# Kernel optimization log

Measured on AMD Instinct MI355X. Metric: run time of the kernel, lower is better.

## Reference

```python
import jax, jax.numpy as jnp
import numpy as np

B, L, S = 32, 8192, 128  # E == S == D == 128 required by the einsum labeling

def setup_inputs() -> dict:
    key = jax.random.key(0)
    kq, kk, kv = jax.random.split(key, 3)
    queries = jax.random.normal(kq, (B, L, S), dtype=jnp.float32)
    keys = jax.random.normal(kk, (B, S, S), dtype=jnp.float32)
    values = jax.random.normal(kv, (B, S, S), dtype=jnp.float32)
    return {"queries": queries, "keys": keys, "values": values}

def reference(queries, keys, values):
    # queries: (B, L, E), keys/values: (B, S, D) with E == S == D.
    # scores_1: sum-pooled outer product term (reduced-rank additive score)
    s1 = queries.sum(-1)[:, :, None] * keys.sum(-1)[:, None, :]   # (B, L, S)
    # scores_2: q contracted against key-position axis (plain batched matmul, no transpose)
    s2 = jnp.einsum('bls,bsd->bld', queries, keys)                # (B, L, S)
    A = jax.nn.softmax(s1 + s2, axis=-1)                          # (B, L, S)
    out = jnp.einsum('bls,bsd->bld', A, values)                   # (B, L, D)
    # original returns shape (B, 1, L, D) for the 3D-input path
    return out[:, None, :, :]
```

## Files before the change

kernel.cpp:

```cpp
#include <hip/hip_runtime.h>

#define SDIM 128
#define LDIM 8192
#define BATCH 32

#define WS_KV_STRIDE 65536
#define WS_KSUM_OFF (BATCH * WS_KV_STRIDE)

typedef __attribute__((ext_vector_type(8))) _Float16 half8;
typedef __attribute__((ext_vector_type(16))) float float16;

union H8U { half8 v; _Float16 h[8]; unsigned w[4]; };
union PU { _Float16 h[2]; unsigned u; };

static __device__ __forceinline__ float16 mfma_f16(half8 a, half8 b, float16 c) {
    return __builtin_amdgcn_mfma_f32_32x32x16_f16(a, b, c, 0, 0, 0);
}

__global__ __launch_bounds__(256) void prep_kernel(
        const float* __restrict__ keys, const float* __restrict__ values,
        char* __restrict__ ws) {
    __shared__ float T[SDIM * SDIM];
    const int b = blockIdx.x >> 1;
    const int which = blockIdx.x & 1;
    const int tid = threadIdx.x;
    const float* src = (which ? values : keys) + (size_t)b * SDIM * SDIM;

    #pragma unroll
    for (int it = 0; it < 16; ++it) {
        int i = tid + it * 256;
        int r = i >> 5, c0 = (i & 31) * 4;
        float4 v = ((const float4*)src)[i];
        float f[4] = {v.x, v.y, v.z, v.w};
        #pragma unroll
        for (int k = 0; k < 4; ++k)
            T[r * SDIM + ((c0 + k + r) & 127)] = f[k];
    }
    __syncthreads();

    if (which == 0 && tid < SDIM) {
        const float4* row = (const float4*)&T[tid * SDIM];
        float s = 0.f;
        #pragma unroll
        for (int i = 0; i < 32; ++i) { float4 v = row[i]; s += v.x + v.y + v.z + v.w; }
        ((float*)(ws + WS_KSUM_OFF + b * 512))[tid] = s;
    }

    char* dst = ws + (size_t)b * WS_KV_STRIDE + (which ? 32768 : 0);
    #pragma unroll
    for (int it = 0; it < 8; ++it) {
        int entry = it * 256 + tid;
        int lane = entry & 63, ln = lane & 31, H = lane >> 5;
        int m = entry >> 9, ks = (entry >> 6) & 7;
        int r = 32 * m + ln;
        int c0 = 16 * ks + 8 * H;
        H8U o;
        #pragma unroll
        for (int i = 0; i < 8; ++i) {
            int c = c0 + i;
            o.h[i] = (_Float16)T[c * SDIM + ((r + c) & 127)];
        }
        *(half8*)(dst + entry * 16) = o.v;
    }
}

__global__ __launch_bounds__(256, 4) void attn_kernel(
        const float* __restrict__ q, const char* __restrict__ ws,
        float* __restrict__ out) {
    __shared__ char smQ[32768];
    __shared__ float qsum_s[SDIM];
    __shared__ float ksum_s[SDIM];
    const int blk = blockIdx.x;
    const int b = blk >> 6, tile = blk & 63;
    const int tid = threadIdx.x, wave = tid >> 6, lane = tid & 63;
    const int H = lane >> 5, ln = lane & 31;

    const char* wsb = ws + (size_t)b * WS_KV_STRIDE;
    const float* qblk = q + ((size_t)b * LDIM + tile * 128) * SDIM;
    float* ob = out + ((size_t)b * LDIM + tile * 128 + wave * 32) * SDIM;

    if (tid < 32)
        ((float4*)ksum_s)[tid] = ((const float4*)(ws + WS_KSUM_OFF + b * 512))[tid];

    {
        float4 bufA[4][2], bufB[4][2];
        #pragma unroll
        for (int it = 0; it < 4; ++it) {
            int idx = it * 256 + tid;
            const float* p = qblk + (idx >> 4) * SDIM + (idx & 15) * 8;
            bufA[it][0] = *(const float4*)p;
            bufA[it][1] = *(const float4*)(p + 4);
        }
        #pragma unroll
        for (int it = 0; it < 4; ++it) {
            int idx = (it + 4) * 256 + tid;
            const float* p = qblk + (idx >> 4) * SDIM + (idx & 15) * 8;
            bufB[it][0] = *(const float4*)p;
            bufB[it][1] = *(const float4*)(p + 4);
        }
        #pragma unroll
        for (int g = 0; g < 2; ++g) {
            #pragma unroll
            for (int it2 = 0; it2 < 4; ++it2) {
                int it = g * 4 + it2;
                int idx = it * 256 + tid;
                int row = idx >> 4, cc = idx & 15;
                float4 v0 = g ? bufB[it2][0] : bufA[it2][0];
                float4 v1 = g ? bufB[it2][1] : bufA[it2][1];
                float f[8] = {v0.x, v0.y, v0.z, v0.w, v1.x, v1.y, v1.z, v1.w};
                float s = f[0] + f[1] + f[2] + f[3] + f[4] + f[5] + f[6] + f[7];
                s += __shfl_xor(s, 1, 64);
                s += __shfl_xor(s, 2, 64);
                s += __shfl_xor(s, 4, 64);
                s += __shfl_xor(s, 8, 64);
                if ((tid & 15) == 0) qsum_s[row] = s;
                H8U hv;
                #pragma unroll
                for (int i = 0; i < 8; ++i) hv.h[i] = (_Float16)f[i];
                *(half8*)(smQ + row * 256 + ((cc ^ (row & 15)) * 16)) = hv.v;
            }
        }
    }
    __syncthreads();

    const char* qrp = smQ + (wave * 32 + ln) * 256;
    const char* ktp = wsb;
    const char* vtp = wsb + 32768;
    const int lo16 = lane * 16;

    float16 acc[4];
    #pragma unroll
    for (int m = 0; m < 4; ++m) acc[m] = (float16)(0.0f);

    half8 ah[2][4];
    #pragma unroll
    for (int m = 0; m < 4; ++m)
        ah[0][m] = *(const half8*)(ktp + (m * 8) * 1024 + lo16);
    #pragma unroll
    for (int ks = 0; ks < 8; ++ks) {
        const int cur = ks & 1, nxt = cur ^ 1;
        if (ks < 7) {
            #pragma unroll
            for (int m = 0; m < 4; ++m)
                ah[nxt][m] = *(const half8*)(ktp + (m * 8 + ks + 1) * 1024 + lo16);
        }
        half8 bh = *(const half8*)(qrp + ((2 * ks + H) ^ (ln & 15)) * 16);
        #pragma unroll
        for (int m = 0; m < 4; ++m) acc[m] = mfma_f16(ah[cur][m], bh, acc[m]);
    }

    half8 av[2][4];
    #pragma unroll
    for (int dm = 0; dm < 4; ++dm)
        av[0][dm] = *(const half8*)(vtp + (dm * 8) * 1024 + lo16);

    const float qs = qsum_s[wave * 32 + ln];
    #pragma unroll
    for (int m = 0; m < 4; ++m)
        #pragma unroll
        for (int g = 0; g < 4; ++g) {
            float4 k4 = *(const float4*)&ksum_s[m * 32 + g * 8 + H * 4];
            acc[m][4 * g + 0] = fmaf(k4.x, qs, acc[m][4 * g + 0]);
            acc[m][4 * g + 1] = fmaf(k4.y, qs, acc[m][4 * g + 1]);
            acc[m][4 * g + 2] = fmaf(k4.z, qs, acc[m][4 * g + 2]);
            acc[m][4 * g + 3] = fmaf(k4.w, qs, acc[m][4 * g + 3]);
        }

    float mx = -1e30f;
    #pragma unroll
    for (int m = 0; m < 4; ++m)
        #pragma unroll
        for (int r = 0; r < 16; ++r) mx = fmaxf(mx, acc[m][r]);
    mx = fmaxf(mx, __shfl_xor(mx, 32, 64));
    float sum = 0.0f;
    #pragma unroll
    for (int m = 0; m < 4; ++m)
        #pragma unroll
        for (int r = 0; r < 16; ++r) {
            float e = __expf(acc[m][r] - mx);
            acc[m][r] = e;
            sum += e;
        }
    sum += __shfl_xor(sum, 32, 64);
    const float inv = 1.0f / sum;

    unsigned pk[4][8];
    #pragma unroll
    for (int m = 0; m < 4; ++m)
        #pragma unroll
        for (int rr = 0; rr < 8; ++rr) {
            PU pu;
            pu.h[0] = (_Float16)(acc[m][2 * rr] * inv);
            pu.h[1] = (_Float16)(acc[m][2 * rr + 1] * inv);
            pk[m][rr] = pu.u;
        }

    float16 oacc[4];
    #pragma unroll
    for (int m = 0; m < 4; ++m) oacc[m] = (float16)(0.0f);

    #pragma unroll
    for (int t = 0; t < 8; ++t) {
        const int cur = t & 1, nxt = cur ^ 1;
        if (t < 7) {
            #pragma unroll
            for (int dm = 0; dm < 4; ++dm)
                av[nxt][dm] = *(const half8*)(vtp + (dm * 8 + t + 1) * 1024 + lo16);
        }
        const int m = t >> 1;
        const int c = 4 * (t & 1);
        unsigned p0 = pk[m][c], p1 = pk[m][c + 1], p2 = pk[m][c + 2], p3 = pk[m][c + 3];
        unsigned a0 = H ? p2 : p0, a1 = H ? p3 : p1;
        unsigned s0 = H ? p0 : p2, s1 = H ? p1 : p3;
        unsigned r0 = (unsigned)__shfl_xor((int)s0, 32, 64);
        unsigned r1 = (unsigned)__shfl_xor((int)s1, 32, 64);
        H8U bf;
        bf.w[0] = H ? r0 : a0;
        bf.w[1] = H ? r1 : a1;
        bf.w[2] = H ? a0 : r0;
        bf.w[3] = H ? a1 : r1;
        #pragma unroll
        for (int dm = 0; dm < 4; ++dm)
            oacc[dm] = mfma_f16(av[cur][dm], bf.v, oacc[dm]);
    }

    #pragma unroll
    for (int dm = 0; dm < 4; ++dm)
        #pragma unroll
        for (int g = 0; g < 4; ++g) {
            float4 v = make_float4(oacc[dm][4 * g], oacc[dm][4 * g + 1],
                                   oacc[dm][4 * g + 2], oacc[dm][4 * g + 3]);
            *(float4*)(ob + ln * SDIM + dm * 32 + g * 8 + H * 4) = v;
        }
}

extern "C" void kernel_launch(void* const* d_in, const int* in_sizes, int n_in,
                              void* d_out, int out_size, void* d_ws, size_t ws_size,
                              hipStream_t stream) {
    const float* q    = (const float*)d_in[0];
    const float* keys = (const float*)d_in[1];
    const float* vals = (const float*)d_in[2];
    float* out = (float*)d_out;
    char*  ws  = (char*)d_ws;

    prep_kernel<<<BATCH * 2, 256, 0, stream>>>(keys, vals, ws);
    attn_kernel<<<BATCH * (LDIM / 128), 256, 0, stream>>>(q, ws, out);
}
```

Before: 268.4 us.

## Split prep into finer blocks, drop attn barrier, deepen K/V prefetch

The prep kernel now runs as 288 blocks: one per 32-column slice of each K or V matrix, plus separate blocks for the key row sums. This is meant to cut the latency of a prep stage that previously used only 64 blocks. In the attention kernel, each wave loads its own 32 Q rows, so the __syncthreads is removed. ksum is read directly from global memory with register prefetch, and the K/V fragment loads are issued two steps ahead so they overlap the MFMAs. The main risks are extra register pressure and a possible cross-wave hazard if any shared Q data is still read by another wave.

```diff
diff --git a/kernel.cpp b/kernel.cpp
--- a/kernel.cpp
+++ b/kernel.cpp
@@ -20,47 +20,50 @@
 __global__ __launch_bounds__(256) void prep_kernel(
         const float* __restrict__ keys, const float* __restrict__ values,
         char* __restrict__ ws) {
-    __shared__ float T[SDIM * SDIM];
-    const int b = blockIdx.x >> 1;
-    const int which = blockIdx.x & 1;
+    __shared__ float T[SDIM * 33];
+    const int blk = blockIdx.x;
     const int tid = threadIdx.x;
-    const float* src = (which ? values : keys) + (size_t)b * SDIM * SDIM;
-
-    #pragma unroll
-    for (int it = 0; it < 16; ++it) {
-        int i = tid + it * 256;
-        int r = i >> 5, c0 = (i & 31) * 4;
-        float4 v = ((const float4*)src)[i];
-        float f[4] = {v.x, v.y, v.z, v.w};
-        #pragma unroll
-        for (int k = 0; k < 4; ++k)
-            T[r * SDIM + ((c0 + k + r) & 127)] = f[k];
-    }
-    __syncthreads();
-
-    if (which == 0 && tid < SDIM) {
-        const float4* row = (const float4*)&T[tid * SDIM];
+
+    if (blk < 256) {
+        const int b = blk >> 3, which = (blk >> 2) & 1, m = blk & 3;
+        const float* src = (which ? values : keys) + (size_t)b * SDIM * SDIM;
+
+        #pragma unroll
+        for (int j = 0; j < 4; ++j) {
+            int lin = j * 256 + tid;
+            int c = lin >> 3, f4 = lin & 7;
+            float4 v = *(const float4*)(src + c * SDIM + m * 32 + f4 * 4);
+            T[c * 33 + f4 * 4 + 0] = v.x;
+            T[c * 33 + f4 * 4 + 1] = v.y;
+            T[c * 33 + f4 * 4 + 2] = v.z;
+            T[c * 33 + f4 * 4 + 3] = v.w;
+        }
+        __syncthreads();
+
+        char* dst = ws + (size_t)b * WS_KV_STRIDE + (which ? 32768 : 0);
+        #pragma unroll
+        for (int j = 0; j < 2; ++j) {
+            int e = j * 256 + tid;
+            int ks = e >> 6, lane = e & 63;
+            int Hh = (lane >> 5) & 1, ln = lane & 31;
+            int c0 = 16 * ks + 8 * Hh;
+            H8U o;
+            #pragma unroll
+            for (int i = 0; i < 8; ++i)
+                o.h[i] = (_Float16)T[(c0 + i) * 33 + ln];
+            *(half8*)(dst + ((m * 8 + ks) * 64 + lane) * 16) = o.v;
+        }
+    } else {
+        const int b = blk - 256;
+        const float* src = keys + (size_t)b * SDIM * SDIM;
+        int row = tid >> 1, h = tid & 1;
+        const float4* p = (const float4*)(src + row * SDIM + h * 64);
         float s = 0.f;
         #pragma unroll
-        for (int i = 0; i < 32; ++i) { float4 v = row[i]; s += v.x + v.y + v.z + v.w; }
-        ((float*)(ws + WS_KSUM_OFF + b * 512))[tid] = s;
-    }
-
-    char* dst = ws + (size_t)b * WS_KV_STRIDE + (which ? 32768 : 0);
-    #pragma unroll
-    for (int it = 0; it < 8; ++it) {
-        int entry = it * 256 + tid;
-        int lane = entry & 63, ln = lane & 31, H = lane >> 5;
-        int m = entry >> 9, ks = (entry >> 6) & 7;
-        int r = 32 * m + ln;
-        int c0 = 16 * ks + 8 * H;
-        H8U o;
-        #pragma unroll
-        for (int i = 0; i < 8; ++i) {
-            int c = c0 + i;
-            o.h[i] = (_Float16)T[c * SDIM + ((r + c) & 127)];
-        }
-        *(half8*)(dst + entry * 16) = o.v;
+        for (int k = 0; k < 16; ++k) { float4 v = p[k]; s += v.x + v.y + v.z + v.w; }
+        s += __shfl_xor(s, 1, 64);
+        if (h == 0)
+            ((float*)(ws + WS_KSUM_OFF + b * 512))[row] = s;
     }
 }
 
@@ -69,7 +72,6 @@
         float* __restrict__ out) {
     __shared__ char smQ[32768];
     __shared__ float qsum_s[SDIM];
-    __shared__ float ksum_s[SDIM];
     const int blk = blockIdx.x;
     const int b = blk >> 6, tile = blk & 63;
     const int tid = threadIdx.x, wave = tid >> 6, lane = tid & 63;
@@ -79,22 +81,23 @@
     const float* qblk = q + ((size_t)b * LDIM + tile * 128) * SDIM;
     float* ob = out + ((size_t)b * LDIM + tile * 128 + wave * 32) * SDIM;
 
-    if (tid < 32)
-        ((float4*)ksum_s)[tid] = ((const float4*)(ws + WS_KSUM_OFF + b * 512))[tid];
-
+    const char* ktp = wsb;
+    const char* vtp = wsb + 32768;
+    const int lo16 = lane * 16;
+
+    const int rb = (wave << 5) + (((tid >> 4) & 3) << 3);
+    const int cc = tid & 15;
     {
         float4 bufA[4][2], bufB[4][2];
         #pragma unroll
         for (int it = 0; it < 4; ++it) {
-            int idx = it * 256 + tid;
-            const float* p = qblk + (idx >> 4) * SDIM + (idx & 15) * 8;
+            const float* p = qblk + (rb + it) * SDIM + cc * 8;
             bufA[it][0] = *(const float4*)p;
             bufA[it][1] = *(const float4*)(p + 4);
         }
         #pragma unroll
         for (int it = 0; it < 4; ++it) {
-            int idx = (it + 4) * 256 + tid;
-            const float* p = qblk + (idx >> 4) * SDIM + (idx & 15) * 8;
+            const float* p = qblk + (rb + 4 + it) * SDIM + cc * 8;
             bufB[it][0] = *(const float4*)p;
             bufB[it][1] = *(const float4*)(p + 4);
         }
@@ -102,9 +105,7 @@
         for (int g = 0; g < 2; ++g) {
             #pragma unroll
             for (int it2 = 0; it2 < 4; ++it2) {
-                int it = g * 4 + it2;
-                int idx = it * 256 + tid;
-                int row = idx >> 4, cc = idx & 15;
+                int row = rb + g * 4 + it2;
                 float4 v0 = g ? bufB[it2][0] : bufA[it2][0];
                 float4 v1 = g ? bufB[it2][1] : bufA[it2][1];
                 float f[8] = {v0.x, v0.y, v0.z, v0.w, v1.x, v1.y, v1.z, v1.w};
@@ -121,33 +122,38 @@
             }
         }
     }
-    __syncthreads();
 
     const char* qrp = smQ + (wave * 32 + ln) * 256;
-    const char* ktp = wsb;
-    const char* vtp = wsb + 32768;
-    const int lo16 = lane * 16;
+
+    half8 ah[2][4];
+    #pragma unroll
+    for (int m = 0; m < 4; ++m)
+        ah[0][m] = *(const half8*)(ktp + (m * 8 + 0) * 1024 + lo16);
+    #pragma unroll
+    for (int m = 0; m < 4; ++m)
+        ah[1][m] = *(const half8*)(ktp + (m * 8 + 1) * 1024 + lo16);
 
     float16 acc[4];
     #pragma unroll
     for (int m = 0; m < 4; ++m) acc[m] = (float16)(0.0f);
 
-    half8 ah[2][4];
-    #pragma unroll
-    for (int m = 0; m < 4; ++m)
-        ah[0][m] = *(const half8*)(ktp + (m * 8) * 1024 + lo16);
     #pragma unroll
     for (int ks = 0; ks < 8; ++ks) {
-        const int cur = ks & 1, nxt = cur ^ 1;
-        if (ks < 7) {
+        const int cur = ks & 1;
+        half8 bh = *(const half8*)(qrp + ((2 * ks + H) ^ (ln & 15)) * 16);
+        #pragma unroll
+        for (int m = 0; m < 4; ++m) acc[m] = mfma_f16(ah[cur][m], bh, acc[m]);
+        if (ks < 6) {
             #pragma unroll
             for (int m = 0; m < 4; ++m)
-                ah[nxt][m] = *(const half8*)(ktp + (m * 8 + ks + 1) * 1024 + lo16);
-        }
-        half8 bh = *(const half8*)(qrp + ((2 * ks + H) ^ (ln & 15)) * 16);
-        #pragma unroll
-        for (int m = 0; m < 4; ++m) acc[m] = mfma_f16(ah[cur][m], bh, acc[m]);
-    }
+                ah[cur][m] = *(const half8*)(ktp + (m * 8 + ks + 2) * 1024 + lo16);
+        }
+    }
+
+    const float4* ksg = (const float4*)(ws + WS_KSUM_OFF + b * 512);
+    float4 kk[2][4];
+    #pragma unroll
+    for (int g = 0; g < 4; ++g) kk[0][g] = ksg[g * 2 + H];
 
     half8 av[2][4];
     #pragma unroll
@@ -156,15 +162,21 @@
 
     const float qs = qsum_s[wave * 32 + ln];
     #pragma unroll
-    for (int m = 0; m < 4; ++m)
+    for (int m = 0; m < 4; ++m) {
+        const int cur = m & 1;
+        if (m < 3) {
+            #pragma unroll
+            for (int g = 0; g < 4; ++g) kk[cur ^ 1][g] = ksg[(m + 1) * 8 + g * 2 + H];
+        }
         #pragma unroll
         for (int g = 0; g < 4; ++g) {
-            float4 k4 = *(const float4*)&ksum_s[m * 32 + g * 8 + H * 4];
+            float4 k4 = kk[cur][g];
             acc[m][4 * g + 0] = fmaf(k4.x, qs, acc[m][4 * g + 0]);
             acc[m][4 * g + 1] = fmaf(k4.y, qs, acc[m][4 * g + 1]);
             acc[m][4 * g + 2] = fmaf(k4.z, qs, acc[m][4 * g + 2]);
             acc[m][4 * g + 3] = fmaf(k4.w, qs, acc[m][4 * g + 3]);
         }
+    }
 
     float mx = -1e30f;
     #pragma unroll
@@ -195,18 +207,17 @@
             pk[m][rr] = pu.u;
         }
 
+    #pragma unroll
+    for (int dm = 0; dm < 4; ++dm)
+        av[1][dm] = *(const half8*)(vtp + (dm * 8 + 1) * 1024 + lo16);
+
     float16 oacc[4];
     #pragma unroll
     for (int m = 0; m < 4; ++m) oacc[m] = (float16)(0.0f);
 
     #pragma unroll
     for (int t = 0; t < 8; ++t) {
-        const int cur = t & 1, nxt = cur ^ 1;
-        if (t < 7) {
-            #pragma unroll
-            for (int dm = 0; dm < 4; ++dm)
-                av[nxt][dm] = *(const half8*)(vtp + (dm * 8 + t + 1) * 1024 + lo16);
-        }
+        const int cur = t & 1;
         const int m = t >> 1;
         const int c = 4 * (t & 1);
         unsigned p0 = pk[m][c], p1 = pk[m][c + 1], p2 = pk[m][c + 2], p3 = pk[m][c + 3];
@@ -222,6 +233,11 @@
         #pragma unroll
         for (int dm = 0; dm < 4; ++dm)
             oacc[dm] = mfma_f16(av[cur][dm], bf.v, oacc[dm]);
+        if (t < 6) {
+            #pragma unroll
+            for (int dm = 0; dm < 4; ++dm)
+                av[cur][dm] = *(const half8*)(vtp + (dm * 8 + t + 2) * 1024 + lo16);
+        }
     }
 
     #pragma unroll
@@ -243,6 +259,6 @@
     float* out = (float*)d_out;
     char*  ws  = (char*)d_ws;
 
-    prep_kernel<<<BATCH * 2, 256, 0, stream>>>(keys, vals, ws);
+    prep_kernel<<<BATCH * 8 + BATCH, 256, 0, stream>>>(keys, vals, ws);
     attn_kernel<<<BATCH * (LDIM / 128), 256, 0, stream>>>(q, ws, out);
 }
```

After: 263.0 us. -2.0%, faster.
